# Kernel tuning notes

Hardware: AMD Instinct MI355X
Metric: run time of the kernel (lower is better)

Reference implementation:

```python
import jax, jax.numpy as jnp
import numpy as np

N_HEAD = 16
THETA = 10000.0


def _rope_cos_sin(T, head_dim):
    # freqs: (T, head_dim//2), matches torch.polar(ones, outer(t, 1/theta^(2i/d)))
    inv = 1.0 / (THETA ** (jnp.arange(0, head_dim, 2, dtype=jnp.float32) / head_dim))
    freqs = jnp.arange(T, dtype=jnp.float32)[:, None] * inv[None, :]
    # broadcast shape (1, T, 1, head_dim//2) over (B, T, H, head_dim//2)
    return jnp.cos(freqs)[None, :, None, :], jnp.sin(freqs)[None, :, None, :]


def _apply_rope(t, cos, sin):
    # t: (B, T, H, hd); pairs (even, odd) form complex numbers
    B, T, H, hd = t.shape
    tr = t.astype(jnp.float32).reshape(B, T, H, hd // 2, 2)
    re, im = tr[..., 0], tr[..., 1]
    out = jnp.stack([re * cos - im * sin, re * sin + im * cos], axis=-1)
    return out.reshape(B, T, H, hd).astype(t.dtype)


def setup_inputs() -> dict:
    key = jax.random.key(0)
    k1, k2, k3 = jax.random.split(key, 3)
    C = 1024
    x = jax.random.normal(k1, (4, 2048, C), dtype=jnp.float32)
    w_attn = jax.random.normal(k2, (3 * C, C), dtype=jnp.float32) * 0.02
    w_proj = jax.random.normal(k3, (C, C), dtype=jnp.float32) * 0.02
    return {"x": x, "w_attn": w_attn, "w_proj": w_proj}


def reference(x, w_attn, w_proj):
    B, T, C = x.shape
    H = N_HEAD
    hd = C // H
    qkv = x @ w_attn.T  # (B, T, 3C) fused QKV projection
    q, k, v = jnp.split(qkv, 3, axis=-1)
    q = q.reshape(B, T, H, hd)
    k = k.reshape(B, T, H, hd)
    v = v.reshape(B, T, H, hd).transpose(0, 2, 1, 3)  # (B, H, T, hd)
    cos, sin = _rope_cos_sin(T, hd)
    q = _apply_rope(q, cos, sin).transpose(0, 2, 1, 3)  # (B, H, T, hd)
    k = _apply_rope(k, cos, sin).transpose(0, 2, 1, 3)
    scale = 1.0 / jnp.sqrt(jnp.float32(hd))
    scores = jnp.einsum('bhqd,bhkd->bhqk', q, k) * scale
    attn = jax.nn.softmax(scores, axis=-1)
    y = jnp.einsum('bhqk,bhkd->bhqd', attn, v)  # (B, H, T, hd)
    y = y.transpose(0, 2, 1, 3).reshape(B, T, C)
    return y @ w_proj.T
```

## Files before the change

### kernel.cpp

```cpp
#include <hip/hip_runtime.h>
#include <math.h>

#define BATCH 4
#define TSEQ 2048
#define CDIM 1024
#define NHEAD 16
#define HDIM 64
#define M_ROWS (BATCH * TSEQ)

typedef float f32x4 __attribute__((ext_vector_type(4)));
typedef __bf16 bf16x8 __attribute__((ext_vector_type(8)));
typedef unsigned int u32x4 __attribute__((ext_vector_type(4)));

typedef const __attribute__((address_space(1))) void gas_void;
typedef __attribute__((address_space(3))) void las_void;

static __device__ __forceinline__ unsigned short f2bf(float f) {
    unsigned int x = __float_as_uint(f);
    x += 0x7fffu + ((x >> 16) & 1u);
    return (unsigned short)(x >> 16);
}

__global__ void prep_kernel(const float* __restrict__ x, unsigned short* __restrict__ xb,
                            const float* __restrict__ wa, unsigned short* __restrict__ wab,
                            const float* __restrict__ wp, unsigned short* __restrict__ wpb,
                            float* __restrict__ cosT, float* __restrict__ sinT) {
    int blk = blockIdx.x;
    if (blk < 6144) {
        const float* in;
        unsigned short* out;
        int base;
        if (blk < 4096)      { in = x;  out = xb;  base = blk; }
        else if (blk < 5632) { in = wa; out = wab; base = blk - 4096; }
        else                 { in = wp; out = wpb; base = blk - 5632; }
        int i = (base * 256 + threadIdx.x) << 3;
        float4 a = *(const float4*)(in + i);
        float4 b = *(const float4*)(in + i + 4);
        union { unsigned short u[8]; u32x4 v; } pk;
        pk.u[0] = f2bf(a.x); pk.u[1] = f2bf(a.y); pk.u[2] = f2bf(a.z); pk.u[3] = f2bf(a.w);
        pk.u[4] = f2bf(b.x); pk.u[5] = f2bf(b.y); pk.u[6] = f2bf(b.z); pk.u[7] = f2bf(b.w);
        *(u32x4*)(out + i) = pk.v;
    } else {
        int idx = (blk - 6144) * 256 + threadIdx.x;
        int t = idx >> 5;
        int i = idx & 31;
        double inv = pow(10000.0, -((double)(2 * i)) / (double)HDIM);
        double ph = (double)t * inv;
        cosT[idx] = (float)cos(ph);
        sinT[idx] = (float)sin(ph);
    }
}

#define GROW(p) (((p) & 64) + (((p) & 15) << 2) + (((p) >> 4) & 3))
#define GEMM_CORE(A_, B_, K_, bm_, bn_)                                          \
    const int tid = threadIdx.x;                                                 \
    const int w = tid >> 6, lane = tid & 63;                                     \
    const int l15 = lane & 15, quad = lane >> 4;                                 \
    const int wm = w >> 1, wn = w & 1;                                           \
    const int srow = (w << 5) + (lane >> 2);                                     \
    const int kpart = (lane & 3) << 3;                                           \
    const int ksw = (((lane & 3) ^ ((lane >> 3) & 3)) << 3);                     \
    const int rsw = (l15 >> 1) & 3;                                              \
    const unsigned short* Ag0 = A_ + (size_t)(bm_ + srow) * K_ + ksw;            \
    const unsigned short* Ag1 = A_ + (size_t)(bm_ + srow + 16) * K_ + ksw;       \
    const unsigned short* Bg0 = B_ + (size_t)(bn_ + GROW(srow)) * K_ + ksw;      \
    const unsigned short* Bg1 = B_ + (size_t)(bn_ + GROW(srow + 16)) * K_ + ksw; \
    unsigned short* Al0 = As + srow * 32 + kpart;                                \
    unsigned short* Al1 = As + (srow + 16) * 32 + kpart;                         \
    unsigned short* Bl0 = Bs + srow * 32 + kpart;                                \
    unsigned short* Bl1 = Bs + (srow + 16) * 32 + kpart;                         \
    f32x4 acc[4][4];                                                             \
    _Pragma("unroll")                                                            \
    for (int i = 0; i < 4; ++i)                                                  \
        _Pragma("unroll")                                                        \
        for (int j = 0; j < 4; ++j) acc[i][j] = (f32x4){0.f, 0.f, 0.f, 0.f};     \
    for (int k0 = 0; k0 < K_; k0 += 32) {                                        \
        __builtin_amdgcn_global_load_lds((gas_void*)(Ag0 + k0), (las_void*)Al0, 16, 0, 0); \
        __builtin_amdgcn_global_load_lds((gas_void*)(Ag1 + k0), (las_void*)Al1, 16, 0, 0); \
        __builtin_amdgcn_global_load_lds((gas_void*)(Bg0 + k0), (las_void*)Bl0, 16, 0, 0); \
        __builtin_amdgcn_global_load_lds((gas_void*)(Bg1 + k0), (las_void*)Bl1, 16, 0, 0); \
        __syncthreads();                                                         \
        bf16x8 af[4], bf[4];                                                     \
        _Pragma("unroll")                                                        \
        for (int mi = 0; mi < 4; ++mi)                                           \
            af[mi] = __builtin_bit_cast(bf16x8,                                  \
                *(const u32x4*)(As + ((wm << 6) + (mi << 4) + l15) * 32 + ((quad ^ rsw) << 3))); \
        _Pragma("unroll")                                                        \
        for (int ni = 0; ni < 4; ++ni)                                           \
            bf[ni] = __builtin_bit_cast(bf16x8,                                  \
                *(const u32x4*)(Bs + ((wn << 6) + (ni << 4) + l15) * 32 + ((quad ^ rsw) << 3))); \
        _Pragma("unroll")                                                        \
        for (int mi = 0; mi < 4; ++mi)                                           \
            _Pragma("unroll")                                                    \
            for (int ni = 0; ni < 4; ++ni)                                       \
                acc[mi][ni] = __builtin_amdgcn_mfma_f32_16x16x32_bf16(af[mi], bf[ni], acc[mi][ni], 0, 0, 0); \
        __syncthreads();                                                         \
    }

__global__ __launch_bounds__(256) void gemm_qkv_fused(
        const unsigned short* __restrict__ A, const unsigned short* __restrict__ B,
        unsigned short* __restrict__ qb, unsigned short* __restrict__ kb,
        unsigned short* __restrict__ vb,
        const float* __restrict__ cosT, const float* __restrict__ sinT) {
    __shared__ __align__(16) unsigned short As[128 * 32];
    __shared__ __align__(16) unsigned short Bs[128 * 32];
    const int bm = blockIdx.y << 7;
    const int bn = blockIdx.x << 7;
    GEMM_CORE(A, B, CDIM, bm, bn)

    const int nbase = bn + (wn << 6);
    const int mbase = bm + (wm << 6);
    const int b = mbase >> 11;
    const int tt0 = mbase & (TSEQ - 1);
    const int d0 = l15 << 2;
    const int fi = l15 << 1;

    if (nbase < 2 * CDIM) {
        const int isQ = (nbase < CDIM) ? 1 : 0;
        unsigned short* dst = isQ ? qb : kb;
        const float qs = isQ ? 0.18033688f : 1.0f;
        const int h = (nbase & (CDIM - 1)) >> 6;
        unsigned short* hb = dst + (size_t)(b * NHEAD + h) * TSEQ * HDIM;
#pragma unroll
        for (int mi = 0; mi < 4; ++mi) {
#pragma unroll
            for (int r = 0; r < 4; ++r) {
                const int t = tt0 + (mi << 4) + (quad << 2) + r;
                float2 cc = *(const float2*)(cosT + (t << 5) + fi);
                float2 ss = *(const float2*)(sinT + (t << 5) + fi);
                float re0 = acc[mi][0][r], im0 = acc[mi][1][r];
                float re1 = acc[mi][2][r], im1 = acc[mi][3][r];
                union { unsigned short u[4]; uint2 v; } pk;
                pk.u[0] = f2bf((re0 * cc.x - im0 * ss.x) * qs);
                pk.u[1] = f2bf((re0 * ss.x + im0 * cc.x) * qs);
                pk.u[2] = f2bf((re1 * cc.y - im1 * ss.y) * qs);
                pk.u[3] = f2bf((re1 * ss.y + im1 * cc.y) * qs);
                *(uint2*)(hb + (size_t)t * HDIM + d0) = pk.v;
            }
        }
    } else {
        const int h = (nbase - 2 * CDIM) >> 6;
        unsigned short* hb = vb + (size_t)(b * NHEAD + h) * HDIM * TSEQ;
#pragma unroll
        for (int mi = 0; mi < 4; ++mi) {
            const int t0 = tt0 + (mi << 4) + (quad << 2);
#pragma unroll
            for (int ni = 0; ni < 4; ++ni) {
                const int d = d0 + ni;
                union { unsigned short u[4]; uint2 v; } pk;
#pragma unroll
                for (int r = 0; r < 4; ++r) pk.u[r] = f2bf(acc[mi][ni][r]);
                *(uint2*)(hb + (size_t)d * TSEQ + t0) = pk.v;
            }
        }
    }
}

__global__ __launch_bounds__(256) void gemm_proj(
        const unsigned short* __restrict__ A, const unsigned short* __restrict__ B,
        float* __restrict__ C) {
    __shared__ __align__(16) unsigned short As[128 * 32];
    __shared__ __align__(16) unsigned short Bs[128 * 32];
    const int bm = blockIdx.y << 7;
    const int bn = blockIdx.x << 7;
    GEMM_CORE(A, B, CDIM, bm, bn)

#pragma unroll
    for (int mi = 0; mi < 4; ++mi)
#pragma unroll
        for (int r = 0; r < 4; ++r) {
            const int row = bm + (wm << 6) + (mi << 4) + (quad << 2) + r;
            float4 v = make_float4(acc[mi][0][r], acc[mi][1][r], acc[mi][2][r], acc[mi][3][r]);
            *(float4*)(C + (size_t)row * CDIM + bn + (wn << 6) + (l15 << 2)) = v;
        }
}

#define KTILE 64
#define NKT (TSEQ / KTILE)
#define QBLK 256
#define SWZ(row, ch) (((row) << 6) + ((((ch) ^ ((row) & 7))) << 3))
__global__ __launch_bounds__(256, 2) void attn_mfma(
        const unsigned short* __restrict__ qb, const unsigned short* __restrict__ kb,
        const unsigned short* __restrict__ vb, unsigned short* __restrict__ y) {
    const int bh = blockIdx.x;
    const int qt = blockIdx.y;
    const int b = bh >> 4, h = bh & 15;
    const int tid  = threadIdx.x;
    const int w    = tid >> 6;
    const int lane = tid & 63;
    const int l15  = lane & 15;
    const int quad = lane >> 4;

    __shared__ __align__(16) unsigned short Ks[2][KTILE * 64];
    __shared__ __align__(16) unsigned short Vs[2][HDIM * 64];

    const size_t qoff = ((size_t)bh * TSEQ + qt * QBLK + w * 64) * HDIM;
    bf16x8 aq[4][2];
#pragma unroll
    for (int ni = 0; ni < 4; ++ni)
#pragma unroll
        for (int kc = 0; kc < 2; ++kc) {
            u32x4 v = *(const u32x4*)(qb + qoff + (size_t)(ni * 16 + l15) * HDIM + kc * 32 + quad * 8);
            aq[ni][kc] = __builtin_bit_cast(bf16x8, v);
        }

    f32x4 o[4][4];
    float l_r[4];
#pragma unroll
    for (int ni = 0; ni < 4; ++ni) {
        l_r[ni] = 0.f;
#pragma unroll
        for (int nc = 0; nc < 4; ++nc) o[ni][nc] = (f32x4){0.f, 0.f, 0.f, 0.f};
    }

    const unsigned short* kbase = kb + (size_t)bh * TSEQ * HDIM;
    const unsigned short* vbase = vb + (size_t)bh * HDIM * TSEQ;

    const int sr = tid >> 3;
    const int s8 = tid & 7;
    const int sp = s8 << 3;
    const int stK0 = SWZ(sr, s8);
    const int stK1 = SWZ(sr + 32, s8);
    const int vrow0 = ((sr & 3) << 4) + (sr >> 2);
    const int vrow1 = vrow0 + 8;
    const int chV  = ((s8 >> 2) << 2) + ((s8 & 1) << 1);
    const int offV = ((s8 >> 1) & 1) << 2;
    const int e0 = vrow0 & 7;
    const int stV00 = (vrow0 << 6) + ((chV ^ e0) << 3) + offV;
    const int stV01 = (vrow0 << 6) + (((chV + 1) ^ e0) << 3) + offV;
    const int stV10 = (vrow1 << 6) + ((chV ^ e0) << 3) + offV;
    const int stV11 = (vrow1 << 6) + (((chV + 1) ^ e0) << 3) + offV;

    u32x4 kr[2], vr[2];
#pragma unroll
    for (int l = 0; l < 2; ++l) {
        int idx = sr + (l << 5);
        kr[l] = *(const u32x4*)(kbase + (size_t)idx * HDIM + sp);
        vr[l] = *(const u32x4*)(vbase + (size_t)idx * TSEQ + sp);
    }
    *(u32x4*)&Ks[0][stK0] = kr[0];
    *(u32x4*)&Ks[0][stK1] = kr[1];
    *(uint2*)&Vs[0][stV00] = make_uint2(vr[0][0], vr[0][1]);
    *(uint2*)&Vs[0][stV01] = make_uint2(vr[0][2], vr[0][3]);
    *(uint2*)&Vs[0][stV10] = make_uint2(vr[1][0], vr[1][1]);
    *(uint2*)&Vs[0][stV11] = make_uint2(vr[1][2], vr[1][3]);
#pragma unroll
    for (int l = 0; l < 2; ++l) {
        int idx = sr + (l << 5);
        kr[l] = *(const u32x4*)(kbase + (size_t)(KTILE + idx) * HDIM + sp);
        vr[l] = *(const u32x4*)(vbase + (size_t)idx * TSEQ + KTILE + sp);
    }

    for (int kt = 0; kt < NKT; ++kt) {
        const int cur = kt & 1;
        __syncthreads();

        bf16x8 ap[4][2];
#pragma unroll
        for (int pvk = 0; pvk < 2; ++pvk) {
            f32x4 s[2][4];
#pragma unroll
            for (int mi2 = 0; mi2 < 2; ++mi2) {
                const int rowK = (pvk * 2 + mi2) * 16 + l15;
                bf16x8 k0 = __builtin_bit_cast(bf16x8, *(const u32x4*)&Ks[cur][SWZ(rowK, quad)]);
                bf16x8 k1 = __builtin_bit_cast(bf16x8, *(const u32x4*)&Ks[cur][SWZ(rowK, quad ^ 4)]);
#pragma unroll
                for (int ni = 0; ni < 4; ++ni) {
                    f32x4 a2 = (f32x4){0.f, 0.f, 0.f, 0.f};
                    a2 = __builtin_amdgcn_mfma_f32_16x16x32_bf16(k0, aq[ni][0], a2, 0, 0, 0);
                    a2 = __builtin_amdgcn_mfma_f32_16x16x32_bf16(k1, aq[ni][1], a2, 0, 0, 0);
                    s[mi2][ni] = a2;
                }
            }
#pragma unroll
            for (int ni = 0; ni < 4; ++ni) {
                float p0[4], p1[4];
#pragma unroll
                for (int r = 0; r < 4; ++r) {
                    p0[r] = __builtin_amdgcn_exp2f(s[0][ni][r]);
                    p1[r] = __builtin_amdgcn_exp2f(s[1][ni][r]);
                }
                l_r[ni] += ((p0[0] + p0[1]) + (p0[2] + p0[3]))
                         + ((p1[0] + p1[1]) + (p1[2] + p1[3]));
                u32x4 pk;
                pk[0] = __builtin_amdgcn_perm(__float_as_uint(p0[1]), __float_as_uint(p0[0]), 0x07060302u);
                pk[1] = __builtin_amdgcn_perm(__float_as_uint(p0[3]), __float_as_uint(p0[2]), 0x07060302u);
                pk[2] = __builtin_amdgcn_perm(__float_as_uint(p1[1]), __float_as_uint(p1[0]), 0x07060302u);
                pk[3] = __builtin_amdgcn_perm(__float_as_uint(p1[3]), __float_as_uint(p1[2]), 0x07060302u);
                ap[ni][pvk] = __builtin_bit_cast(bf16x8, pk);
            }
        }

        if (kt + 1 < NKT) {
            const int nxt = cur ^ 1;
            *(u32x4*)&Ks[nxt][stK0] = kr[0];
            *(u32x4*)&Ks[nxt][stK1] = kr[1];
            *(uint2*)&Vs[nxt][stV00] = make_uint2(vr[0][0], vr[0][1]);
            *(uint2*)&Vs[nxt][stV01] = make_uint2(vr[0][2], vr[0][3]);
            *(uint2*)&Vs[nxt][stV10] = make_uint2(vr[1][0], vr[1][1]);
            *(uint2*)&Vs[nxt][stV11] = make_uint2(vr[1][2], vr[1][3]);
            if (kt + 2 < NKT) {
                int base = (kt + 2) * KTILE;
#pragma unroll
                for (int l = 0; l < 2; ++l) {
                    int idx = sr + (l << 5);
                    kr[l] = *(const u32x4*)(kbase + (size_t)(base + idx) * HDIM + sp);
                    vr[l] = *(const u32x4*)(vbase + (size_t)idx * TSEQ + base + sp);
                }
            }
        }

#pragma unroll
        for (int nc = 0; nc < 4; ++nc) {
            const int rowV = nc * 16 + l15;
#pragma unroll
            for (int kc = 0; kc < 2; ++kc) {
                bf16x8 bv = __builtin_bit_cast(bf16x8,
                    *(const u32x4*)&Vs[cur][SWZ(rowV, (kc << 2) + quad)]);
#pragma unroll
                for (int ni = 0; ni < 4; ++ni)
                    o[ni][nc] = __builtin_amdgcn_mfma_f32_16x16x32_bf16(ap[ni][kc], bv, o[ni][nc], 0, 0, 0);
            }
        }
    }

#pragma unroll
    for (int ni = 0; ni < 4; ++ni) {
        l_r[ni] += __shfl_xor(l_r[ni], 16, 64);
        l_r[ni] += __shfl_xor(l_r[ni], 32, 64);
    }
    const int srcl = (quad << 4) + (quad << 2);
#pragma unroll
    for (int ni = 0; ni < 4; ++ni)
#pragma unroll
        for (int r = 0; r < 4; ++r) {
            float inv_l = 1.f / __shfl(l_r[ni], srcl + r, 64);
            int t = qt * QBLK + w * 64 + ni * 16 + quad * 4 + r;
            unsigned short* row = y + (size_t)(b * TSEQ + t) * CDIM + h * HDIM;
            union { unsigned short u[4]; uint2 v; } pk;
#pragma unroll
            for (int nc = 0; nc < 4; ++nc) pk.u[nc] = f2bf(o[ni][nc][r] * inv_l);
            *(uint2*)(row + (l15 << 2)) = pk.v;
        }
}

extern "C" void kernel_launch(void* const* d_in, const int* in_sizes, int n_in,
                              void* d_out, int out_size, void* d_ws, size_t ws_size,
                              hipStream_t stream) {
    const float* x      = (const float*)d_in[0];
    const float* w_attn = (const float*)d_in[1];
    const float* w_proj = (const float*)d_in[2];
    float* out = (float*)d_out;

    unsigned short* xb  = (unsigned short*)d_ws;
    unsigned short* wab = xb  + (size_t)M_ROWS * CDIM;
    unsigned short* wpb = wab + (size_t)3 * CDIM * CDIM;
    unsigned short* qb  = wpb + (size_t)CDIM * CDIM;
    unsigned short* kb  = qb  + (size_t)BATCH * NHEAD * TSEQ * HDIM;
    unsigned short* vb  = kb  + (size_t)BATCH * NHEAD * TSEQ * HDIM;
    unsigned short* yb  = vb  + (size_t)BATCH * NHEAD * TSEQ * HDIM;
    float* cosT = (float*)(yb + (size_t)M_ROWS * CDIM);
    float* sinT = cosT + TSEQ * (HDIM / 2);

    prep_kernel<<<6400, 256, 0, stream>>>(x, xb, w_attn, wab, w_proj, wpb, cosT, sinT);

    dim3 g1(3 * CDIM / 128, M_ROWS / 128);
    gemm_qkv_fused<<<g1, 256, 0, stream>>>(xb, wab, qb, kb, vb, cosT, sinT);

    dim3 g2(BATCH * NHEAD, TSEQ / QBLK);
    attn_mfma<<<g2, 256, 0, stream>>>(qb, kb, vb, yb);

    dim3 g3(CDIM / 128, M_ROWS / 128);
    gemm_proj<<<g3, 256, 0, stream>>>(yb, wpb, out);
}
```

Measured before the change: 261.5 us.

## Triple-buffer GEMM LDS tiles with async global_load_lds prefetch two stages ahead

Replaces the single-buffered K loop in both projection GEMMs with a 3-stage LDS ring. Loads for tile t+2 are issued before computing tile t, and a partial vmcnt wait with a single barrier replaces the two syncthreads per iteration. This is meant to hide global memory latency behind MFMA work. It triples LDS use per block (48KB), which may lower occupancy, and it relies on the vmcnt counts being correct for memory ordering.

```diff
diff --git a/kernel.cpp b/kernel.cpp
--- a/kernel.cpp
+++ b/kernel.cpp
@@ -52,6 +52,13 @@
 }
 
 #define GROW(p) (((p) & 64) + (((p) & 15) << 2) + (((p) >> 4) & 3))
+#define GEMM_STAGE(bufo, kofs)                                                   \
+    do {                                                                         \
+        __builtin_amdgcn_global_load_lds((gas_void*)(Ag0 + (kofs)), (las_void*)(Al0 + (bufo)), 16, 0, 0); \
+        __builtin_amdgcn_global_load_lds((gas_void*)(Ag1 + (kofs)), (las_void*)(Al1 + (bufo)), 16, 0, 0); \
+        __builtin_amdgcn_global_load_lds((gas_void*)(Bg0 + (kofs)), (las_void*)(Bl0 + (bufo)), 16, 0, 0); \
+        __builtin_amdgcn_global_load_lds((gas_void*)(Bg1 + (kofs)), (las_void*)(Bl1 + (bufo)), 16, 0, 0); \
+    } while (0)
 #define GEMM_CORE(A_, B_, K_, bm_, bn_)                                          \
     const int tid = threadIdx.x;                                                 \
     const int w = tid >> 6, lane = tid & 63;                                     \
@@ -74,27 +81,36 @@
     for (int i = 0; i < 4; ++i)                                                  \
         _Pragma("unroll")                                                        \
         for (int j = 0; j < 4; ++j) acc[i][j] = (f32x4){0.f, 0.f, 0.f, 0.f};     \
-    for (int k0 = 0; k0 < K_; k0 += 32) {                                        \
-        __builtin_amdgcn_global_load_lds((gas_void*)(Ag0 + k0), (las_void*)Al0, 16, 0, 0); \
-        __builtin_amdgcn_global_load_lds((gas_void*)(Ag1 + k0), (las_void*)Al1, 16, 0, 0); \
-        __builtin_amdgcn_global_load_lds((gas_void*)(Bg0 + k0), (las_void*)Bl0, 16, 0, 0); \
-        __builtin_amdgcn_global_load_lds((gas_void*)(Bg1 + k0), (las_void*)Bl1, 16, 0, 0); \
-        __syncthreads();                                                         \
-        bf16x8 af[4], bf[4];                                                     \
-        _Pragma("unroll")                                                        \
-        for (int mi = 0; mi < 4; ++mi)                                           \
-            af[mi] = __builtin_bit_cast(bf16x8,                                  \
-                *(const u32x4*)(As + ((wm << 6) + (mi << 4) + l15) * 32 + ((quad ^ rsw) << 3))); \
-        _Pragma("unroll")                                                        \
-        for (int ni = 0; ni < 4; ++ni)                                           \
-            bf[ni] = __builtin_bit_cast(bf16x8,                                  \
-                *(const u32x4*)(Bs + ((wn << 6) + (ni << 4) + l15) * 32 + ((quad ^ rsw) << 3))); \
-        _Pragma("unroll")                                                        \
-        for (int mi = 0; mi < 4; ++mi)                                           \
+    {                                                                            \
+        const int NT = K_ / 32;                                                  \
+        GEMM_STAGE(0, 0);                                                        \
+        GEMM_STAGE(4096, 32);                                                    \
+        int cur = 0;                                                             \
+        for (int t = 0; t < NT; ++t) {                                           \
+            if (t < NT - 1) asm volatile("s_waitcnt vmcnt(4) lgkmcnt(0)\n\ts_barrier" ::: "memory"); \
+            else            asm volatile("s_waitcnt vmcnt(0) lgkmcnt(0)\n\ts_barrier" ::: "memory"); \
+            if (t + 2 < NT) {                                                    \
+                int nxt = cur + 2; if (nxt >= 3) nxt -= 3;                       \
+                GEMM_STAGE(nxt * 4096, (t + 2) * 32);                            \
+            }                                                                    \
+            const unsigned short* Ab = As + cur * 4096;                          \
+            const unsigned short* Bb = Bs + cur * 4096;                          \
+            bf16x8 af[4], bf[4];                                                 \
+            _Pragma("unroll")                                                    \
+            for (int mi = 0; mi < 4; ++mi)                                       \
+                af[mi] = __builtin_bit_cast(bf16x8,                              \
+                    *(const u32x4*)(Ab + ((wm << 6) + (mi << 4) + l15) * 32 + ((quad ^ rsw) << 3))); \
             _Pragma("unroll")                                                    \
             for (int ni = 0; ni < 4; ++ni)                                       \
-                acc[mi][ni] = __builtin_amdgcn_mfma_f32_16x16x32_bf16(af[mi], bf[ni], acc[mi][ni], 0, 0, 0); \
-        __syncthreads();                                                         \
+                bf[ni] = __builtin_bit_cast(bf16x8,                              \
+                    *(const u32x4*)(Bb + ((wn << 6) + (ni << 4) + l15) * 32 + ((quad ^ rsw) << 3))); \
+            _Pragma("unroll")                                                    \
+            for (int mi = 0; mi < 4; ++mi)                                       \
+                _Pragma("unroll")                                                \
+                for (int ni = 0; ni < 4; ++ni)                                   \
+                    acc[mi][ni] = __builtin_amdgcn_mfma_f32_16x16x32_bf16(af[mi], bf[ni], acc[mi][ni], 0, 0, 0); \
+            ++cur; if (cur == 3) cur = 0;                                        \
+        }                                                                        \
     }
 
 __global__ __launch_bounds__(256) void gemm_qkv_fused(
@@ -102,8 +118,8 @@
         unsigned short* __restrict__ qb, unsigned short* __restrict__ kb,
         unsigned short* __restrict__ vb,
         const float* __restrict__ cosT, const float* __restrict__ sinT) {
-    __shared__ __align__(16) unsigned short As[128 * 32];
-    __shared__ __align__(16) unsigned short Bs[128 * 32];
+    __shared__ __align__(16) unsigned short As[3 * 128 * 32];
+    __shared__ __align__(16) unsigned short Bs[3 * 128 * 32];
     const int bm = blockIdx.y << 7;
     const int bn = blockIdx.x << 7;
     GEMM_CORE(A, B, CDIM, bm, bn)
@@ -159,8 +175,8 @@
 __global__ __launch_bounds__(256) void gemm_proj(
         const unsigned short* __restrict__ A, const unsigned short* __restrict__ B,
         float* __restrict__ C) {
-    __shared__ __align__(16) unsigned short As[128 * 32];
-    __shared__ __align__(16) unsigned short Bs[128 * 32];
+    __shared__ __align__(16) unsigned short As[3 * 128 * 32];
+    __shared__ __align__(16) unsigned short Bs[3 * 128 * 32];
     const int bm = blockIdx.y << 7;
     const int bn = blockIdx.x << 7;
     GEMM_CORE(A, B, CDIM, bm, bn)
```

Measured after the change: 269.3 us. 1.03x slower.
